# Performance work log

Measured on AMD Instinct MI355X. Metric: run time of the kernel, lower is better.

## Reference

```python
import jax, jax.numpy as jnp
import numpy as np

N, E, G = 32768, 262144, 1024
FIN, ED = 32, 8
H, C = 4, 64            # gat_heads, graph_hidden_dim
HC = H * C              # 256
FP_IN, DESC_IN = 2048, 200
GOUT, FPOUT, DOUT = 64, 256, 64
TIN = GOUT + FPOUT + DOUT  # 384
NT = 12
BN_EPS = 1e-5


def bn_eval(x, gamma, beta):
    # eval-mode BatchNorm1d with default running stats (mean=0, var=1)
    inv = 1.0 / jnp.sqrt(1.0 + BN_EPS)
    return x * (gamma * inv) + beta


def gatv2(x, edge_index, edge_attr, Wl, bl, Wr, br, We, att, bias):
    """PyG GATv2Conv (concat heads, add_self_loops=True, fill_value='mean')."""
    n = x.shape[0]
    src, dst = edge_index[0], edge_index[1]
    # self-loop edge_attr = mean of incoming edge_attr per node (PyG fill_value='mean')
    deg = jax.ops.segment_sum(jnp.ones(src.shape, x.dtype), dst, n)
    ea_loop = jax.ops.segment_sum(edge_attr, dst, n) / jnp.maximum(deg, 1.0)[:, None]
    loop = jnp.arange(n)
    src = jnp.concatenate([src, loop])
    dst = jnp.concatenate([dst, loop])
    ea = jnp.concatenate([edge_attr, ea_loop], axis=0)
    xl = (x @ Wl + bl).reshape(n, H, C)   # source transform
    xr = (x @ Wr + br).reshape(n, H, C)   # target transform
    ee = (ea @ We).reshape(-1, H, C)      # edge transform (no bias in PyG)
    m = jax.nn.leaky_relu(xl[src] + xr[dst] + ee, 0.2)  # [E', H, C]
    logit = jnp.einsum('ehc,hc->eh', m, att)            # [E', H]
    # segment softmax over incoming edges of each target node
    lmax = jax.ops.segment_max(logit, dst, n)
    p = jnp.exp(logit - lmax[dst])
    alpha = p / jax.ops.segment_sum(p, dst, n)[dst]
    out = jax.ops.segment_sum(xl[src] * alpha[:, :, None], dst, n)  # [n, H, C]
    return out.reshape(n, HC) + bias


def setup_inputs() -> dict:
    key = jax.random.key(0)
    ks = iter(jax.random.split(key, 64))

    def p(shape, scale=0.05):
        return jax.random.normal(next(ks), shape, dtype=jnp.float32) * scale

    inp = {}
    inp['x'] = jax.random.normal(next(ks), (N, FIN), dtype=jnp.float32)
    inp['edge_index'] = jax.random.randint(next(ks), (2, E), 0, N, dtype=jnp.int32)
    inp['edge_attr'] = jax.random.normal(next(ks), (E, ED), dtype=jnp.float32)
    inp['batch'] = (jnp.arange(N) * G) // N          # sorted, covers all G graphs
    inp['fp'] = jax.random.uniform(next(ks), (G, FP_IN), dtype=jnp.float32)
    inp['desc'] = jax.random.normal(next(ks), (G, DESC_IN), dtype=jnp.float32)
    # GATv2 layer 1 (in=FIN) and layer 2 (in=HC)
    for tag, fin in (('c1', FIN), ('c2', HC)):
        inp[tag + '_Wl'] = p((fin, HC))
        inp[tag + '_bl'] = p((HC,))
        inp[tag + '_Wr'] = p((fin, HC))
        inp[tag + '_br'] = p((HC,))
        inp[tag + '_We'] = p((ED, HC))
        inp[tag + '_att'] = p((H, C))
        inp[tag + '_bias'] = p((HC,))
    inp['gW'], inp['gb'] = p((HC, GOUT)), p((GOUT,))
    inp['g_gn'], inp['g_bt'] = jnp.ones((GOUT,)), jnp.zeros((GOUT,))
    inp['fW'], inp['fb'] = p((FP_IN, FPOUT)), p((FPOUT,))
    inp['f_gn'], inp['f_bt'] = jnp.ones((FPOUT,)), jnp.zeros((FPOUT,))
    inp['dW'], inp['db'] = p((DESC_IN, DOUT)), p((DOUT,))
    inp['d_gn'], inp['d_bt'] = jnp.ones((DOUT,)), jnp.zeros((DOUT,))
    inp['k1W'], inp['k1b'] = p((TIN, TIN // 2)), p((TIN // 2,))
    inp['k1_gn'], inp['k1_bt'] = jnp.ones((TIN // 2,)), jnp.zeros((TIN // 2,))
    inp['k2W'], inp['k2b'] = p((TIN // 2, TIN // 4)), p((TIN // 4,))
    inp['k2_gn'], inp['k2_bt'] = jnp.ones((TIN // 4,)), jnp.zeros((TIN // 4,))
    inp['k3W'], inp['k3b'] = p((TIN // 4, NT)), p((NT,))
    return inp


def reference(x, edge_index, edge_attr, batch, fp, desc,
              c1_Wl, c1_bl, c1_Wr, c1_br, c1_We, c1_att, c1_bias,
              c2_Wl, c2_bl, c2_Wr, c2_br, c2_We, c2_att, c2_bias,
              gW, gb, g_gn, g_bt, fW, fb, f_gn, f_bt, dW, db, d_gn, d_bt,
              k1W, k1b, k1_gn, k1_bt, k2W, k2b, k2_gn, k2_bt, k3W, k3b):
    h = jax.nn.relu(gatv2(x, edge_index, edge_attr, c1_Wl, c1_bl, c1_Wr, c1_br, c1_We, c1_att, c1_bias))
    h = jax.nn.relu(gatv2(h, edge_index, edge_attr, c2_Wl, c2_bl, c2_Wr, c2_br, c2_We, c2_att, c2_bias))
    xg = jax.ops.segment_max(h, batch, G)                 # global_max_pool
    xg = bn_eval(jax.nn.relu(xg @ gW + gb), g_gn, g_bt)
    xf = bn_eval(jax.nn.relu(fp @ fW + fb), f_gn, f_bt)
    xd = bn_eval(jax.nn.relu(desc @ dW + db), d_gn, d_bt)
    z = jnp.concatenate([xg, xf, xd], axis=1)             # [G, TIN]
    z = bn_eval(jax.nn.relu(z @ k1W + k1b), k1_gn, k1_bt)  # dropout off (eval)
    z = bn_eval(jax.nn.relu(z @ k2W + k2b), k2_gn, k2_bt)
    return z @ k3W + k3b                                  # [G, NT]
```

## Files before the change

### kernel.cpp

```cpp
#include <hip/hip_runtime.h>
#include <hip/hip_bf16.h>
#include <math.h>

#define NHEAD 4
#define HC 256

typedef short short8 __attribute__((ext_vector_type(8)));
typedef short short4v __attribute__((ext_vector_type(4)));
typedef float f32x4 __attribute__((ext_vector_type(4)));

__device__ inline f32x4 bf4_to_f32(short4v v)
{
  f32x4 r;
#pragma unroll
  for (int i = 0; i < 4; ++i)
    r[i] = __uint_as_float(((unsigned)(unsigned short)v[i]) << 16);
  return r;
}

__device__ inline float bf_to_f32(unsigned short u)
{
  return __uint_as_float(((unsigned)u) << 16);
}

template <int CTRL>
__device__ inline float dpp_radd(float x)
{
  int yi = __builtin_amdgcn_update_dpp(0, __float_as_int(x), CTRL, 0xf, 0xf, true);
  return x + __int_as_float(yi);
}

__global__ void prep_kernel(
    const float* __restrict__ x, const float* __restrict__ fp,
    const float* __restrict__ c1Wl, const float* __restrict__ c1Wr,
    const float* __restrict__ c2Wl, const float* __restrict__ c2Wr,
    const float* __restrict__ desc, const float* __restrict__ dW,
    const float* __restrict__ k1W,
    const int* __restrict__ dst, int* __restrict__ deg,
    __hip_bfloat16* __restrict__ xbf, __hip_bfloat16* __restrict__ fpbf,
    __hip_bfloat16* __restrict__ wt1, __hip_bfloat16* __restrict__ wt2,
    __hip_bfloat16* __restrict__ descbf, __hip_bfloat16* __restrict__ dwt,
    __hip_bfloat16* __restrict__ k1wt,
    int N, int G, int E, int DIN)
{
  const int n0 = N * 32, n1 = G * 2048, n2 = 512 * 32, n3 = 512 * 256;
  const int n4 = G * 224, n5 = 64 * 224, n6 = 192 * 384;
  int idx = blockIdx.x * 256 + threadIdx.x;
  if (idx < n0) { xbf[idx] = __float2bfloat16(x[idx]); return; }
  idx -= n0;
  if (idx < n1) { fpbf[idx] = __float2bfloat16(fp[idx]); return; }
  idx -= n1;
  if (idx < n2) {
    int n = idx / 32, k = idx - n * 32;
    float v = (n < 256) ? c1Wl[k * 256 + n] : c1Wr[k * 256 + (n - 256)];
    wt1[idx] = __float2bfloat16(v); return;
  }
  idx -= n2;
  if (idx < n3) {
    int n = idx / 256, k = idx - n * 256;
    float v = (n < 256) ? c2Wl[k * 256 + n] : c2Wr[k * 256 + (n - 256)];
    wt2[idx] = __float2bfloat16(v); return;
  }
  idx -= n3;
  if (idx < n4) {
    int row = idx / 224, kp = idx - row * 224;
    float v = (kp < DIN) ? desc[(long)row * DIN + kp] : 0.f;
    descbf[idx] = __float2bfloat16(v); return;
  }
  idx -= n4;
  if (idx < n5) {
    int n = idx / 224, kp = idx - n * 224;
    float v = (kp < DIN) ? dW[kp * 64 + n] : 0.f;
    dwt[idx] = __float2bfloat16(v); return;
  }
  idx -= n5;
  if (idx < n6) {
    int n = idx / 384, k = idx - n * 384;
    k1wt[idx] = __float2bfloat16(k1W[k * 192 + n]); return;
  }
  idx -= n6;
  if (idx < E) atomicAdd(&deg[dst[idx]], 1);
}

__global__ __launch_bounds__(256) void transpose_fwt_kernel(
    const float* __restrict__ fW, __hip_bfloat16* __restrict__ fwt)
{
  __shared__ float tile[64][65];
  int bk = blockIdx.x * 64, bn = blockIdx.y * 64;
  int tx = threadIdx.x & 63, ty = threadIdx.x >> 6;
#pragma unroll
  for (int j = 0; j < 16; ++j) {
    int kl = ty + j * 4;
    tile[kl][tx] = fW[(long)(bk + kl) * 256 + bn + tx];
  }
  __syncthreads();
#pragma unroll
  for (int j = 0; j < 16; ++j) {
    int nl = ty + j * 4;
    fwt[(long)(bn + nl) * 2048 + bk + tx] = __float2bfloat16(tile[tx][nl]);
  }
}

__global__ __launch_bounds__(256) void gemm_mfma_kernel(
    const __hip_bfloat16* __restrict__ A, const __hip_bfloat16* __restrict__ BT,
    const float* __restrict__ bl, const float* __restrict__ br,
    __hip_bfloat16* __restrict__ XL, __hip_bfloat16* __restrict__ XR, int M, int K)
{
  __shared__ short As[128 * 40];
  __shared__ short Bs[128 * 40];
  int bm = blockIdx.x * 128, bn = blockIdx.y * 128;
  int t = threadIdx.x;
  int w = t >> 6, l = t & 63;
  int quad = l >> 4, l16 = l & 15;
  int srow = t >> 1, scol = (t & 1) * 16;

  f32x4 acc[2][8];
#pragma unroll
  for (int i = 0; i < 2; ++i)
#pragma unroll
    for (int j = 0; j < 8; ++j) acc[i][j] = (f32x4){0.f, 0.f, 0.f, 0.f};

  for (int k0 = 0; k0 < K; k0 += 32) {
    *(short8*)&As[srow * 40 + scol] =
        *(const short8*)(const void*)&A[(long)(bm + srow) * K + k0 + scol];
    *(short8*)&As[srow * 40 + scol + 8] =
        *(const short8*)(const void*)&A[(long)(bm + srow) * K + k0 + scol + 8];
    *(short8*)&Bs[srow * 40 + scol] =
        *(const short8*)(const void*)&BT[(long)(bn + srow) * K + k0 + scol];
    *(short8*)&Bs[srow * 40 + scol + 8] =
        *(const short8*)(const void*)&BT[(long)(bn + srow) * K + k0 + scol + 8];
    __syncthreads();
    short8 af[2], bf[8];
#pragma unroll
    for (int mt = 0; mt < 2; ++mt)
      af[mt] = *(short8*)&As[(w * 32 + mt * 16 + l16) * 40 + quad * 8];
#pragma unroll
    for (int nt = 0; nt < 8; ++nt)
      bf[nt] = *(short8*)&Bs[(nt * 16 + l16) * 40 + quad * 8];
#pragma unroll
    for (int mt = 0; mt < 2; ++mt)
#pragma unroll
      for (int nt = 0; nt < 8; ++nt)
        acc[mt][nt] = __builtin_amdgcn_mfma_f32_16x16x32_bf16(af[mt], bf[nt], acc[mt][nt], 0, 0, 0);
    __syncthreads();
  }
#pragma unroll
  for (int mt = 0; mt < 2; ++mt)
#pragma unroll
    for (int nt = 0; nt < 8; ++nt) {
      int col = bn + nt * 16 + l16;
      float b = (col < 256) ? bl[col] : br[col - 256];
#pragma unroll
      for (int r = 0; r < 4; ++r) {
        int row = bm + w * 32 + mt * 16 + quad * 4 + r;
        float v = acc[mt][nt][r] + b;
        if (col < 256)
          XL[(long)row * 256 + col] = __float2bfloat16(v);
        else
          XR[(long)row * 256 + (col - 256)] = __float2bfloat16(v);
      }
    }
}

__global__ __launch_bounds__(256) void gemm_rb_kernel(
    const __hip_bfloat16* __restrict__ A, const __hip_bfloat16* __restrict__ BT,
    const float* __restrict__ bias, const float* __restrict__ gamma,
    const float* __restrict__ beta, void* __restrict__ out,
    int M, int K, int ldc, int coloff, int obf)
{
  __shared__ short As[64 * 40];
  __shared__ short Bs[64 * 40];
  int bm = blockIdx.x * 64, bn = blockIdx.y * 64;
  int t = threadIdx.x;
  int w = t >> 6, l = t & 63;
  int quad = l >> 4, l16 = l & 15;
  int lrow = t >> 2, col8 = (t & 3) * 8;

  f32x4 acc[4];
#pragma unroll
  for (int nt = 0; nt < 4; ++nt) acc[nt] = (f32x4){0.f, 0.f, 0.f, 0.f};

  for (int k0 = 0; k0 < K; k0 += 32) {
    *(short8*)&As[lrow * 40 + col8] =
        *(const short8*)(const void*)&A[(long)(bm + lrow) * K + k0 + col8];
    *(short8*)&Bs[lrow * 40 + col8] =
        *(const short8*)(const void*)&BT[(long)(bn + lrow) * K + k0 + col8];
    __syncthreads();
    short8 af = *(short8*)&As[(w * 16 + l16) * 40 + quad * 8];
#pragma unroll
    for (int nt = 0; nt < 4; ++nt) {
      short8 bf = *(short8*)&Bs[(nt * 16 + l16) * 40 + quad * 8];
      acc[nt] = __builtin_amdgcn_mfma_f32_16x16x32_bf16(af, bf, acc[nt], 0, 0, 0);
    }
    __syncthreads();
  }
  const float inv = rsqrtf(1.f + 1e-5f);
#pragma unroll
  for (int nt = 0; nt < 4; ++nt) {
    int col = bn + nt * 16 + l16;
    float b = bias[col], gm = gamma[col] * inv, bt = beta[col];
#pragma unroll
    for (int r = 0; r < 4; ++r) {
      int row = bm + w * 16 + quad * 4 + r;
      float v = fmaxf(acc[nt][r] + b, 0.f) * gm + bt;
      if (obf)
        ((__hip_bfloat16*)out)[(long)row * ldc + coloff + col] = __float2bfloat16(v);
      else
        ((float*)out)[(long)row * ldc + coloff + col] = v;
    }
  }
}

__global__ __launch_bounds__(256) void gemm_skb_kernel(
    const __hip_bfloat16* __restrict__ A, const __hip_bfloat16* __restrict__ BT,
    float* __restrict__ P, int M, int N, int K, int Kc)
{
  __shared__ short As[64 * 40];
  __shared__ short Bs[64 * 40];
  int bm = blockIdx.x * 64, bn = blockIdx.y * 64;
  int s = blockIdx.z;
  int kb = s * Kc, ke = kb + Kc;
  int t = threadIdx.x;
  int w = t >> 6, l = t & 63;
  int quad = l >> 4, l16 = l & 15;
  int lrow = t >> 2, col8 = (t & 3) * 8;

  f32x4 acc[4];
#pragma unroll
  for (int nt = 0; nt < 4; ++nt) acc[nt] = (f32x4){0.f, 0.f, 0.f, 0.f};

  for (int k0 = kb; k0 < ke; k0 += 32) {
    *(short8*)&As[lrow * 40 + col8] =
        *(const short8*)(const void*)&A[(long)(bm + lrow) * K + k0 + col8];
    *(short8*)&Bs[lrow * 40 + col8] =
        *(const short8*)(const void*)&BT[(long)(bn + lrow) * K + k0 + col8];
    __syncthreads();
    short8 af = *(short8*)&As[(w * 16 + l16) * 40 + quad * 8];
#pragma unroll
    for (int nt = 0; nt < 4; ++nt) {
      short8 bf = *(short8*)&Bs[(nt * 16 + l16) * 40 + quad * 8];
      acc[nt] = __builtin_amdgcn_mfma_f32_16x16x32_bf16(af, bf, acc[nt], 0, 0, 0);
    }
    __syncthreads();
  }
#pragma unroll
  for (int nt = 0; nt < 4; ++nt) {
    int col = bn + nt * 16 + l16;
#pragma unroll
    for (int r = 0; r < 4; ++r) {
      int row = bm + w * 16 + quad * 4 + r;
      P[((long)s * M + row) * N + col] = acc[nt][r];
    }
  }
}

__global__ __launch_bounds__(256) void fp_epilogue_kernel(
    const float* __restrict__ P, const float* __restrict__ bias,
    const float* __restrict__ gamma, const float* __restrict__ beta,
    __hip_bfloat16* __restrict__ zbuf, int M, int N, int S)
{
  int idx = blockIdx.x * 256 + threadIdx.x;
  if (idx >= M * N) return;
  int row = idx / N, col = idx - row * N;
  float v = 0.f;
  for (int s = 0; s < S; ++s) v += P[(long)s * M * N + idx];
  const float inv = rsqrtf(1.f + 1e-5f);
  v = fmaxf(v + bias[col], 0.f) * (gamma[col] * inv) + beta[col];
  zbuf[(long)row * 384 + 64 + col] = __float2bfloat16(v);
}

__global__ __launch_bounds__(256) void poolg_kernel(
    const __hip_bfloat16* __restrict__ h, const float* __restrict__ gW,
    const float* __restrict__ gb, const float* __restrict__ g_gn,
    const float* __restrict__ g_bt, __hip_bfloat16* __restrict__ zbuf, int npg)
{
  __shared__ float smax[256];
  __shared__ float sred[256];
  int g = blockIdx.x, t = threadIdx.x;
  const __hip_bfloat16* base = h + (long)g * npg * HC + t;
  float m = -INFINITY;
#pragma unroll 4
  for (int i = 0; i < npg; ++i)
    m = fmaxf(m, bf_to_f32(*(const unsigned short*)&base[(long)i * HC]));
  smax[t] = m;
  __syncthreads();
  int j = t >> 2, part = t & 3;
  float sum = 0.f;
#pragma unroll 4
  for (int k = part * 64; k < part * 64 + 64; ++k)
    sum = fmaf(smax[k], gW[k * 64 + j], sum);
  sred[t] = sum;
  __syncthreads();
  if (t < 64) {
    float v = sred[t * 4] + sred[t * 4 + 1] + sred[t * 4 + 2] + sred[t * 4 + 3];
    const float inv = rsqrtf(1.f + 1e-5f);
    v = fmaxf(v + gb[t], 0.f) * (g_gn[t] * inv) + g_bt[t];
    zbuf[(long)g * 384 + t] = __float2bfloat16(v);
  }
}

__global__ __launch_bounds__(256) void head23_kernel(
    const float* __restrict__ z1, const float* __restrict__ k2W,
    const float* __restrict__ k2b, const float* __restrict__ k2_gn,
    const float* __restrict__ k2_bt, const float* __restrict__ k3W,
    const float* __restrict__ k3b, float* __restrict__ out)
{
  __shared__ float s1[16 * 192];
  __shared__ float s2[16 * 96];
  int b = blockIdx.x, t = threadIdx.x;
  for (int i = t; i < 16 * 192; i += 256) s1[i] = z1[(long)b * 16 * 192 + i];
  __syncthreads();
  const float inv = rsqrtf(1.f + 1e-5f);
#pragma unroll
  for (int j = 0; j < 6; ++j) {
    int idx = j * 256 + t;
    int row = idx / 96, col = idx - row * 96;
    float acc = 0.f;
#pragma unroll 4
    for (int k = 0; k < 192; ++k) acc = fmaf(s1[row * 192 + k], k2W[k * 96 + col], acc);
    acc = fmaxf(acc + k2b[col], 0.f);
    s2[idx] = acc * (k2_gn[col] * inv) + k2_bt[col];
  }
  __syncthreads();
  if (t < 192) {
    int row = t / 12, col = t - row * 12;
    float acc = 0.f;
#pragma unroll 4
    for (int k = 0; k < 96; ++k) acc = fmaf(s2[row * 96 + k], k3W[k * 12 + col], acc);
    out[(long)(b * 16 + row) * 12 + col] = acc + k3b[col];
  }
}

__global__ __launch_bounds__(1024) void scan1_kernel(
    const int* __restrict__ deg, int* __restrict__ ptr,
    int* __restrict__ bsum, int N)
{
  __shared__ int s[1024];
  int b = blockIdx.x, t = threadIdx.x;
  int i = b * 1024 + t;
  int v = (i < N) ? deg[i] : 0;
  s[t] = v;
  __syncthreads();
  for (int off = 1; off < 1024; off <<= 1) {
    int x = (t >= off) ? s[t - off] : 0;
    __syncthreads();
    s[t] += x;
    __syncthreads();
  }
  if (i < N) ptr[i] = s[t] - v;
  if (t == 1023) bsum[b] = s[1023];
}

__global__ __launch_bounds__(256) void scan2_kernel(
    const int* __restrict__ bsum, int* __restrict__ ptr,
    int* __restrict__ cursor, int N, int nb)
{
  int i = blockIdx.x * 256 + threadIdx.x;
  if (i > N) return;
  if (i == N) {
    int tot = 0;
    for (int j = 0; j < nb; ++j) tot += bsum[j];
    ptr[N] = tot;
    return;
  }
  int b = i >> 10;
  int offv = 0;
  for (int j = 0; j < b; ++j) offv += bsum[j];
  int v = ptr[i] + offv;
  ptr[i] = v;
  cursor[i] = v;
}

__global__ void fill_kernel(const int* __restrict__ src, const int* __restrict__ dst,
                            const float* __restrict__ ea, int* __restrict__ cursor,
                            int* __restrict__ csr_src, float* __restrict__ csr_ea, int E)
{
  int e = blockIdx.x * blockDim.x + threadIdx.x;
  if (e < E) {
    int pos = atomicAdd(&cursor[dst[e]], 1);
    csr_src[pos] = src[e];
    f32x4 a0 = *(const f32x4*)(const void*)&ea[(long)e * 8];
    f32x4 a1 = *(const f32x4*)(const void*)&ea[(long)e * 8 + 4];
    *(f32x4*)&csr_ea[(long)pos * 8] = a0;
    *(f32x4*)&csr_ea[(long)pos * 8 + 4] = a1;
  }
}

__global__ __launch_bounds__(256) void eamean_kernel(
    const float* __restrict__ csr_ea, const int* __restrict__ csr_ptr,
    float* __restrict__ ea_mean, int N)
{
  int idx = blockIdx.x * 256 + threadIdx.x;
  if (idx >= N * 8) return;
  int node = idx >> 3, d = idx & 7;
  int p0 = csr_ptr[node], p1 = csr_ptr[node + 1];
  float s = 0.f;
  for (int k = p0; k < p1; ++k) s += csr_ea[(long)k * 8 + d];
  int cnt = p1 - p0;
  ea_mean[idx] = s / (float)(cnt > 1 ? cnt : 1);
}

__global__ __launch_bounds__(128) void gat_kernel(
    const __hip_bfloat16* __restrict__ xlb, const __hip_bfloat16* __restrict__ xrb,
    const float* __restrict__ csr_ea, const int* __restrict__ csr_src,
    const int* __restrict__ csr_ptr, const float* __restrict__ ea_mean,
    const float* __restrict__ We, const float* __restrict__ att,
    const float* __restrict__ bias, __hip_bfloat16* __restrict__ out, int N)
{
  int lane = threadIdx.x & 63;
  int node = blockIdx.x * 2 + (threadIdx.x >> 6);
  if (node >= N) return;
  int cbase = (lane >> 4) * 64 + (lane & 15) * 4;

  f32x4 attv = *(const f32x4*)(const void*)&att[cbase];
  f32x4 xriv = bf4_to_f32(*(const short4v*)(const void*)&xrb[(long)node * HC + cbase]);
  f32x4 WeR[8];
#pragma unroll
  for (int d = 0; d < 8; ++d)
    WeR[d] = *(const f32x4*)(const void*)&We[d * HC + cbase];

  float rsumA = 0.f, rsumB = 0.f;
  f32x4 accA = (f32x4){0.f, 0.f, 0.f, 0.f};
  f32x4 accB = (f32x4){0.f, 0.f, 0.f, 0.f};

  int p0 = csr_ptr[node], p1 = csr_ptr[node + 1];

  auto edge_compute = [&](f32x4 xls, f32x4 ea0, f32x4 ea1,
                          float& rsum, f32x4& acc) {
    f32x4 mv = xriv + xls;
#pragma unroll
    for (int d = 0; d < 4; ++d) mv += WeR[d] * ea0[d];
#pragma unroll
    for (int d = 0; d < 4; ++d) mv += WeR[d + 4] * ea1[d];
    float t = 0.f;
#pragma unroll
    for (int r = 0; r < 4; ++r) {
      float m = mv[r];
      m = (m > 0.f) ? m : 0.2f * m;
      t = fmaf(m, attv[r], t);
    }
    t = dpp_radd<0x121>(t);
    t = dpp_radd<0x122>(t);
    t = dpp_radd<0x124>(t);
    t = dpp_radd<0x128>(t);
    float p = __expf(t);
    rsum += p;
    acc += p * xls;
  };

  short4v xA = (short4v){0, 0, 0, 0}, xB = xA, xC = xA;
  f32x4 a0A = (f32x4){0.f, 0.f, 0.f, 0.f}, a1A = a0A;
  f32x4 a0B = a0A, a1B = a0A, a0C = a0A, a1C = a0A;
  if (p0 < p1) {
    int s = csr_src[p0];
    a0A = *(const f32x4*)(const void*)&csr_ea[(long)p0 * 8];
    a1A = *(const f32x4*)(const void*)&csr_ea[(long)p0 * 8 + 4];
    xA = *(const short4v*)(const void*)&xlb[(long)s * HC + cbase];
  }
  if (p0 + 1 < p1) {
    int s = csr_src[p0 + 1];
    a0B = *(const f32x4*)(const void*)&csr_ea[(long)(p0 + 1) * 8];
    a1B = *(const f32x4*)(const void*)&csr_ea[(long)(p0 + 1) * 8 + 4];
    xB = *(const short4v*)(const void*)&xlb[(long)s * HC + cbase];
  }
  if (p0 + 2 < p1) {
    int s = csr_src[p0 + 2];
    a0C = *(const f32x4*)(const void*)&csr_ea[(long)(p0 + 2) * 8];
    a1C = *(const f32x4*)(const void*)&csr_ea[(long)(p0 + 2) * 8 + 4];
    xC = *(const short4v*)(const void*)&xlb[(long)s * HC + cbase];
  }
  int k = p0;
  for (; k + 3 <= p1; k += 3) {
    f32x4 e0 = a0A, e1 = a1A;
    short4v xc = xA;
    if (k + 3 < p1) {
      int s = csr_src[k + 3];
      a0A = *(const f32x4*)(const void*)&csr_ea[(long)(k + 3) * 8];
      a1A = *(const f32x4*)(const void*)&csr_ea[(long)(k + 3) * 8 + 4];
      xA = *(const short4v*)(const void*)&xlb[(long)s * HC + cbase];
    }
    edge_compute(bf4_to_f32(xc), e0, e1, rsumA, accA);

    e0 = a0B; e1 = a1B; xc = xB;
    if (k + 4 < p1) {
      int s = csr_src[k + 4];
      a0B = *(const f32x4*)(const void*)&csr_ea[(long)(k + 4) * 8];
      a1B = *(const f32x4*)(const void*)&csr_ea[(long)(k + 4) * 8 + 4];
      xB = *(const short4v*)(const void*)&xlb[(long)s * HC + cbase];
    }
    edge_compute(bf4_to_f32(xc), e0, e1, rsumB, accB);

    e0 = a0C; e1 = a1C; xc = xC;
    if (k + 5 < p1) {
      int s = csr_src[k + 5];
      a0C = *(const f32x4*)(const void*)&csr_ea[(long)(k + 5) * 8];
      a1C = *(const f32x4*)(const void*)&csr_ea[(long)(k + 5) * 8 + 4];
      xC = *(const short4v*)(const void*)&xlb[(long)s * HC + cbase];
    }
    edge_compute(bf4_to_f32(xc), e0, e1, rsumA, accA);
  }
  if (k < p1)     edge_compute(bf4_to_f32(xA), a0A, a1A, rsumA, accA);
  if (k + 1 < p1) edge_compute(bf4_to_f32(xB), a0B, a1B, rsumB, accB);

  f32x4 em0 = *(const f32x4*)(const void*)&ea_mean[(long)node * 8];
  f32x4 em1 = *(const f32x4*)(const void*)&ea_mean[(long)node * 8 + 4];
  f32x4 xls_self = bf4_to_f32(*(const short4v*)(const void*)&xlb[(long)node * HC + cbase]);
  edge_compute(xls_self, em0, em1, rsumB, accB);

  float invs = 1.f / (rsumA + rsumB);
  f32x4 biasv = *(const f32x4*)(const void*)&bias[cbase];
  short4v pk;
#pragma unroll
  for (int r = 0; r < 4; ++r) {
    float v = fmaxf((accA[r] + accB[r]) * invs + biasv[r], 0.f);
    __hip_bfloat16 hv = __float2bfloat16(v);
    pk[r] = *(short*)&hv;
  }
  *(short4v*)&out[(long)node * HC + cbase] = pk;
}

extern "C" void kernel_launch(void* const* d_in, const int* in_sizes, int n_in,
                              void* d_out, int out_size, void* d_ws, size_t ws_size,
                              hipStream_t stream)
{
  const float* x          = (const float*)d_in[0];
  const int*   edge_index = (const int*)d_in[1];
  const float* edge_attr  = (const float*)d_in[2];
  const float* fp         = (const float*)d_in[4];
  const float* desc       = (const float*)d_in[5];
  const float *c1_Wl = (const float*)d_in[6],  *c1_bl = (const float*)d_in[7],
              *c1_Wr = (const float*)d_in[8],  *c1_br = (const float*)d_in[9],
              *c1_We = (const float*)d_in[10], *c1_att = (const float*)d_in[11],
              *c1_bias = (const float*)d_in[12];
  const float *c2_Wl = (const float*)d_in[13], *c2_bl = (const float*)d_in[14],
              *c2_Wr = (const float*)d_in[15], *c2_br = (const float*)d_in[16],
              *c2_We = (const float*)d_in[17], *c2_att = (const float*)d_in[18],
              *c2_bias = (const float*)d_in[19];
  const float *gW = (const float*)d_in[20], *gb = (const float*)d_in[21],
              *g_gn = (const float*)d_in[22], *g_bt = (const float*)d_in[23];
  const float *fW = (const float*)d_in[24], *fb = (const float*)d_in[25],
              *f_gn = (const float*)d_in[26], *f_bt = (const float*)d_in[27];
  const float *dW = (const float*)d_in[28], *db = (const float*)d_in[29],
              *d_gn = (const float*)d_in[30], *d_bt = (const float*)d_in[31];
  const float *k1W = (const float*)d_in[32], *k1b = (const float*)d_in[33],
              *k1_gn = (const float*)d_in[34], *k1_bt = (const float*)d_in[35];
  const float *k2W = (const float*)d_in[36], *k2b = (const float*)d_in[37],
              *k2_gn = (const float*)d_in[38], *k2_bt = (const float*)d_in[39];
  const float *k3W = (const float*)d_in[40], *k3b = (const float*)d_in[41];

  const int N = in_sizes[0] / 32;
  const int E = in_sizes[1] / 2;
  const int G = in_sizes[4] / 2048;
  const int FIN = 32, FPIN = 2048;
  const int DIN = in_sizes[5] / G;

  char* ws = (char*)d_ws;
  size_t off = 0;
  auto alloc = [&](size_t bytes) {
    void* p = ws + off;
    off = (off + bytes + 255) & ~(size_t)255;
    return p;
  };
  __hip_bfloat16* xlb    = (__hip_bfloat16*)alloc((size_t)N * HC * 2);
  __hip_bfloat16* xrb    = (__hip_bfloat16*)alloc((size_t)N * HC * 2);
  __hip_bfloat16* hb1    = (__hip_bfloat16*)alloc((size_t)N * HC * 2);
  __hip_bfloat16* hb2    = (__hip_bfloat16*)alloc((size_t)N * HC * 2);
  __hip_bfloat16* xbf    = (__hip_bfloat16*)alloc((size_t)N * FIN * 2);
  __hip_bfloat16* fpbf   = (__hip_bfloat16*)alloc((size_t)G * FPIN * 2);
  __hip_bfloat16* wt1    = (__hip_bfloat16*)alloc((size_t)512 * FIN * 2);
  __hip_bfloat16* wt2    = (__hip_bfloat16*)alloc((size_t)512 * HC * 2);
  __hip_bfloat16* fwt    = (__hip_bfloat16*)alloc((size_t)256 * FPIN * 2);
  __hip_bfloat16* descbf = (__hip_bfloat16*)alloc((size_t)G * 224 * 2);
  __hip_bfloat16* dwt    = (__hip_bfloat16*)alloc((size_t)64 * 224 * 2);
  __hip_bfloat16* k1wt   = (__hip_bfloat16*)alloc((size_t)192 * 384 * 2);
  __hip_bfloat16* zbuf   = (__hip_bfloat16*)alloc((size_t)G * 384 * 2);
  float* z1      = (float*)alloc((size_t)G * 192 * 4);
  float* P_fp    = (float*)alloc((size_t)4 * G * 256 * 4);
  int*   deg     = (int*)alloc((size_t)N * 4);
  int*   csr_ptr = (int*)alloc((size_t)(N + 1) * 4);
  int*   cursor  = (int*)alloc((size_t)N * 4);
  int*   csr_src = (int*)alloc((size_t)E * 4);
  float* csr_ea  = (float*)alloc((size_t)E * 8 * 4);
  float* ea_mean = (float*)alloc((size_t)N * 8 * 4);
  int*   bsum    = (int*)alloc((size_t)64 * 4);
  (void)ws_size;

  const int* srcp = edge_index;
  const int* dstp = edge_index + E;
  const int nb = (N + 1023) / 1024;

  hipMemsetAsync(deg, 0, (size_t)N * 4, stream);

  {
    long total = (long)N * FIN + (long)G * FPIN + 512 * 32 + 512 * 256 +
                 (long)G * 224 + 64 * 224 + 192 * 384 + E;
    prep_kernel<<<(int)((total + 255) / 256), 256, 0, stream>>>(
        x, fp, c1_Wl, c1_Wr, c2_Wl, c2_Wr, desc, dW, k1W, dstp, deg,
        xbf, fpbf, wt1, wt2, descbf, dwt, k1wt, N, G, E, DIN);
  }
  transpose_fwt_kernel<<<dim3(2048 / 64, 256 / 64), 256, 0, stream>>>(fW, fwt);
  scan1_kernel<<<nb, 1024, 0, stream>>>(deg, csr_ptr, bsum, N);
  scan2_kernel<<<(N + 1 + 255) / 256, 256, 0, stream>>>(bsum, csr_ptr, cursor, N, nb);
  fill_kernel<<<(E + 255) / 256, 256, 0, stream>>>(srcp, dstp, edge_attr, cursor,
                                                   csr_src, csr_ea, E);
  eamean_kernel<<<(N * 8 + 255) / 256, 256, 0, stream>>>(csr_ea, csr_ptr, ea_mean, N);

  gemm_skb_kernel<<<dim3(G / 64, 4, 4), 256, 0, stream>>>(fpbf, fwt, P_fp,
                                                          G, 256, FPIN, FPIN / 4);
  fp_epilogue_kernel<<<(G * 256 + 255) / 256, 256, 0, stream>>>(P_fp, fb, f_gn, f_bt,
                                                                zbuf, G, 256, 4);
  gemm_rb_kernel<<<dim3(G / 64, 1), 256, 0, stream>>>(descbf, dwt, db, d_gn, d_bt,
                                                      zbuf, G, 224, 384, 320, 1);

  gemm_mfma_kernel<<<dim3(N / 128, 4), 256, 0, stream>>>(xbf, wt1, c1_bl, c1_br, xlb, xrb, N, FIN);
  gat_kernel<<<N / 2, 128, 0, stream>>>(xlb, xrb, csr_ea, csr_src, csr_ptr, ea_mean,
                                        c1_We, c1_att, c1_bias, hb1, N);
  gemm_mfma_kernel<<<dim3(N / 128, 4), 256, 0, stream>>>(hb1, wt2, c2_bl, c2_br, xlb, xrb, N, HC);
  gat_kernel<<<N / 2, 128, 0, stream>>>(xlb, xrb, csr_ea, csr_src, csr_ptr, ea_mean,
                                        c2_We, c2_att, c2_bias, hb2, N);

  poolg_kernel<<<G, 256, 0, stream>>>(hb2, gW, gb, g_gn, g_bt, zbuf, N / G);

  gemm_rb_kernel<<<dim3(G / 64, 3), 256, 0, stream>>>(zbuf, k1wt, k1b, k1_gn, k1_bt,
                                                      z1, G, 384, 192, 0, 0);
  head23_kernel<<<G / 16, 256, 0, stream>>>(z1, k2W, k2b, k2_gn, k2_bt, k3W, k3b,
                                            (float*)d_out);
}
```

Before: 450.4 us.

## Process two nodes per wavefront in GAT and fold edge-attr mean into fill

```diff
diff --git a/kernel.cpp b/kernel.cpp
--- a/kernel.cpp
+++ b/kernel.cpp
@@ -373,60 +373,60 @@
 
 __global__ void fill_kernel(const int* __restrict__ src, const int* __restrict__ dst,
                             const float* __restrict__ ea, int* __restrict__ cursor,
-                            int* __restrict__ csr_src, float* __restrict__ csr_ea, int E)
+                            int* __restrict__ csr_src, float* __restrict__ csr_ea,
+                            float* __restrict__ ea_sum, int E)
 {
   int e = blockIdx.x * blockDim.x + threadIdx.x;
   if (e < E) {
-    int pos = atomicAdd(&cursor[dst[e]], 1);
+    int d = dst[e];
+    int pos = atomicAdd(&cursor[d], 1);
     csr_src[pos] = src[e];
     f32x4 a0 = *(const f32x4*)(const void*)&ea[(long)e * 8];
     f32x4 a1 = *(const f32x4*)(const void*)&ea[(long)e * 8 + 4];
     *(f32x4*)&csr_ea[(long)pos * 8] = a0;
     *(f32x4*)&csr_ea[(long)pos * 8 + 4] = a1;
-  }
-}
-
-__global__ __launch_bounds__(256) void eamean_kernel(
-    const float* __restrict__ csr_ea, const int* __restrict__ csr_ptr,
-    float* __restrict__ ea_mean, int N)
-{
-  int idx = blockIdx.x * 256 + threadIdx.x;
-  if (idx >= N * 8) return;
-  int node = idx >> 3, d = idx & 7;
-  int p0 = csr_ptr[node], p1 = csr_ptr[node + 1];
-  float s = 0.f;
-  for (int k = p0; k < p1; ++k) s += csr_ea[(long)k * 8 + d];
-  int cnt = p1 - p0;
-  ea_mean[idx] = s / (float)(cnt > 1 ? cnt : 1);
+#pragma unroll
+    for (int i = 0; i < 4; ++i) atomicAdd(&ea_sum[(long)d * 8 + i], a0[i]);
+#pragma unroll
+    for (int i = 0; i < 4; ++i) atomicAdd(&ea_sum[(long)d * 8 + 4 + i], a1[i]);
+  }
 }
 
 __global__ __launch_bounds__(128) void gat_kernel(
     const __hip_bfloat16* __restrict__ xlb, const __hip_bfloat16* __restrict__ xrb,
     const float* __restrict__ csr_ea, const int* __restrict__ csr_src,
-    const int* __restrict__ csr_ptr, const float* __restrict__ ea_mean,
+    const int* __restrict__ csr_ptr, const float* __restrict__ ea_sum,
     const float* __restrict__ We, const float* __restrict__ att,
     const float* __restrict__ bias, __hip_bfloat16* __restrict__ out, int N)
 {
   int lane = threadIdx.x & 63;
-  int node = blockIdx.x * 2 + (threadIdx.x >> 6);
-  if (node >= N) return;
+  int nodeX = blockIdx.x * 4 + (threadIdx.x >> 6) * 2;
+  int nodeY = nodeX + 1;
   int cbase = (lane >> 4) * 64 + (lane & 15) * 4;
 
+  int p0X = csr_ptr[nodeX], p0Y = csr_ptr[nodeY], p1Y = csr_ptr[nodeY + 1];
+  int degX = p0Y - p0X, degY = p1Y - p0Y;
+
+  short4v xXA = (short4v){0, 0, 0, 0}, xXB = xXA, xYA = xXA, xYB = xXA;
+  if (degX > 0) xXA = *(const short4v*)(const void*)&xlb[(long)csr_src[p0X] * HC + cbase];
+  if (degY > 0) xYA = *(const short4v*)(const void*)&xlb[(long)csr_src[p0Y] * HC + cbase];
+  if (degX > 1) xXB = *(const short4v*)(const void*)&xlb[(long)csr_src[p0X + 1] * HC + cbase];
+  if (degY > 1) xYB = *(const short4v*)(const void*)&xlb[(long)csr_src[p0Y + 1] * HC + cbase];
+
   f32x4 attv = *(const f32x4*)(const void*)&att[cbase];
-  f32x4 xriv = bf4_to_f32(*(const short4v*)(const void*)&xrb[(long)node * HC + cbase]);
+  f32x4 xrivX = bf4_to_f32(*(const short4v*)(const void*)&xrb[(long)nodeX * HC + cbase]);
+  f32x4 xrivY = bf4_to_f32(*(const short4v*)(const void*)&xrb[(long)nodeY * HC + cbase]);
   f32x4 WeR[8];
 #pragma unroll
   for (int d = 0; d < 8; ++d)
     WeR[d] = *(const f32x4*)(const void*)&We[d * HC + cbase];
 
-  float rsumA = 0.f, rsumB = 0.f;
-  f32x4 accA = (f32x4){0.f, 0.f, 0.f, 0.f};
-  f32x4 accB = (f32x4){0.f, 0.f, 0.f, 0.f};
-
-  int p0 = csr_ptr[node], p1 = csr_ptr[node + 1];
-
-  auto edge_compute = [&](f32x4 xls, f32x4 ea0, f32x4 ea1,
-                          float& rsum, f32x4& acc) {
+  float rsumX = 0.f, rsumY = 0.f;
+  f32x4 accX = (f32x4){0.f, 0.f, 0.f, 0.f};
+  f32x4 accY = (f32x4){0.f, 0.f, 0.f, 0.f};
+
+  auto ec = [&](f32x4 xriv, f32x4 xls, f32x4 ea0, f32x4 ea1,
+                float& rsum, f32x4& acc) {
     f32x4 mv = xriv + xls;
 #pragma unroll
     for (int d = 0; d < 4; ++d) mv += WeR[d] * ea0[d];
@@ -448,75 +448,84 @@
     acc += p * xls;
   };
 
-  short4v xA = (short4v){0, 0, 0, 0}, xB = xA, xC = xA;
-  f32x4 a0A = (f32x4){0.f, 0.f, 0.f, 0.f}, a1A = a0A;
-  f32x4 a0B = a0A, a1B = a0A, a0C = a0A, a1C = a0A;
-  if (p0 < p1) {
-    int s = csr_src[p0];
-    a0A = *(const f32x4*)(const void*)&csr_ea[(long)p0 * 8];
-    a1A = *(const f32x4*)(const void*)&csr_ea[(long)p0 * 8 + 4];
-    xA = *(const short4v*)(const void*)&xlb[(long)s * HC + cbase];
-  }
-  if (p0 + 1 < p1) {
-    int s = csr_src[p0 + 1];
-    a0B = *(const f32x4*)(const void*)&csr_ea[(long)(p0 + 1) * 8];
-    a1B = *(const f32x4*)(const void*)&csr_ea[(long)(p0 + 1) * 8 + 4];
-    xB = *(const short4v*)(const void*)&xlb[(long)s * HC + cbase];
-  }
-  if (p0 + 2 < p1) {
-    int s = csr_src[p0 + 2];
-    a0C = *(const f32x4*)(const void*)&csr_ea[(long)(p0 + 2) * 8];
-    a1C = *(const f32x4*)(const void*)&csr_ea[(long)(p0 + 2) * 8 + 4];
-    xC = *(const short4v*)(const void*)&xlb[(long)s * HC + cbase];
-  }
-  int k = p0;
-  for (; k + 3 <= p1; k += 3) {
-    f32x4 e0 = a0A, e1 = a1A;
-    short4v xc = xA;
-    if (k + 3 < p1) {
-      int s = csr_src[k + 3];
-      a0A = *(const f32x4*)(const void*)&csr_ea[(long)(k + 3) * 8];
-      a1A = *(const f32x4*)(const void*)&csr_ea[(long)(k + 3) * 8 + 4];
-      xA = *(const short4v*)(const void*)&xlb[(long)s * HC + cbase];
-    }
-    edge_compute(bf4_to_f32(xc), e0, e1, rsumA, accA);
-
-    e0 = a0B; e1 = a1B; xc = xB;
-    if (k + 4 < p1) {
-      int s = csr_src[k + 4];
-      a0B = *(const f32x4*)(const void*)&csr_ea[(long)(k + 4) * 8];
-      a1B = *(const f32x4*)(const void*)&csr_ea[(long)(k + 4) * 8 + 4];
-      xB = *(const short4v*)(const void*)&xlb[(long)s * HC + cbase];
-    }
-    edge_compute(bf4_to_f32(xc), e0, e1, rsumB, accB);
-
-    e0 = a0C; e1 = a1C; xc = xC;
-    if (k + 5 < p1) {
-      int s = csr_src[k + 5];
-      a0C = *(const f32x4*)(const void*)&csr_ea[(long)(k + 5) * 8];
-      a1C = *(const f32x4*)(const void*)&csr_ea[(long)(k + 5) * 8 + 4];
-      xC = *(const short4v*)(const void*)&xlb[(long)s * HC + cbase];
-    }
-    edge_compute(bf4_to_f32(xc), e0, e1, rsumA, accA);
-  }
-  if (k < p1)     edge_compute(bf4_to_f32(xA), a0A, a1A, rsumA, accA);
-  if (k + 1 < p1) edge_compute(bf4_to_f32(xB), a0B, a1B, rsumB, accB);
-
-  f32x4 em0 = *(const f32x4*)(const void*)&ea_mean[(long)node * 8];
-  f32x4 em1 = *(const f32x4*)(const void*)&ea_mean[(long)node * 8 + 4];
-  f32x4 xls_self = bf4_to_f32(*(const short4v*)(const void*)&xlb[(long)node * HC + cbase]);
-  edge_compute(xls_self, em0, em1, rsumB, accB);
-
-  float invs = 1.f / (rsumA + rsumB);
+  int dmax = degX > degY ? degX : degY;
+  int i = 0;
+  for (; i + 2 <= dmax; i += 2) {
+    if (i < degX) {
+      f32x4 e0 = *(const f32x4*)(const void*)&csr_ea[(long)(p0X + i) * 8];
+      f32x4 e1 = *(const f32x4*)(const void*)&csr_ea[(long)(p0X + i) * 8 + 4];
+      short4v xc = xXA;
+      if (i + 2 < degX)
+        xXA = *(const short4v*)(const void*)&xlb[(long)csr_src[p0X + i + 2] * HC + cbase];
+      ec(xrivX, bf4_to_f32(xc), e0, e1, rsumX, accX);
+    }
+    if (i < degY) {
+      f32x4 e0 = *(const f32x4*)(const void*)&csr_ea[(long)(p0Y + i) * 8];
+      f32x4 e1 = *(const f32x4*)(const void*)&csr_ea[(long)(p0Y + i) * 8 + 4];
+      short4v xc = xYA;
+      if (i + 2 < degY)
+        xYA = *(const short4v*)(const void*)&xlb[(long)csr_src[p0Y + i + 2] * HC + cbase];
+      ec(xrivY, bf4_to_f32(xc), e0, e1, rsumY, accY);
+    }
+    if (i + 1 < degX) {
+      f32x4 e0 = *(const f32x4*)(const void*)&csr_ea[(long)(p0X + i + 1) * 8];
+      f32x4 e1 = *(const f32x4*)(const void*)&csr_ea[(long)(p0X + i + 1) * 8 + 4];
+      short4v xc = xXB;
+      if (i + 3 < degX)
+        xXB = *(const short4v*)(const void*)&xlb[(long)csr_src[p0X + i + 3] * HC + cbase];
+      ec(xrivX, bf4_to_f32(xc), e0, e1, rsumX, accX);
+    }
+    if (i + 1 < degY) {
+      f32x4 e0 = *(const f32x4*)(const void*)&csr_ea[(long)(p0Y + i + 1) * 8];
+      f32x4 e1 = *(const f32x4*)(const void*)&csr_ea[(long)(p0Y + i + 1) * 8 + 4];
+      short4v xc = xYB;
+      if (i + 3 < degY)
+        xYB = *(const short4v*)(const void*)&xlb[(long)csr_src[p0Y + i + 3] * HC + cbase];
+      ec(xrivY, bf4_to_f32(xc), e0, e1, rsumY, accY);
+    }
+  }
+  if (dmax & 1) {
+    if (i < degX) {
+      f32x4 e0 = *(const f32x4*)(const void*)&csr_ea[(long)(p0X + i) * 8];
+      f32x4 e1 = *(const f32x4*)(const void*)&csr_ea[(long)(p0X + i) * 8 + 4];
+      ec(xrivX, bf4_to_f32(xXA), e0, e1, rsumX, accX);
+    }
+    if (i < degY) {
+      f32x4 e0 = *(const f32x4*)(const void*)&csr_ea[(long)(p0Y + i) * 8];
+      f32x4 e1 = *(const f32x4*)(const void*)&csr_ea[(long)(p0Y + i) * 8 + 4];
+      ec(xrivY, bf4_to_f32(xYA), e0, e1, rsumY, accY);
+    }
+  }
+
+  {
+    float invdX = 1.f / (float)(degX > 1 ? degX : 1);
+    f32x4 em0 = *(const f32x4*)(const void*)&ea_sum[(long)nodeX * 8];
+    f32x4 em1 = *(const f32x4*)(const void*)&ea_sum[(long)nodeX * 8 + 4];
+    f32x4 xs = bf4_to_f32(*(const short4v*)(const void*)&xlb[(long)nodeX * HC + cbase]);
+    ec(xrivX, xs, em0 * invdX, em1 * invdX, rsumX, accX);
+  }
+  {
+    float invdY = 1.f / (float)(degY > 1 ? degY : 1);
+    f32x4 em0 = *(const f32x4*)(const void*)&ea_sum[(long)nodeY * 8];
+    f32x4 em1 = *(const f32x4*)(const void*)&ea_sum[(long)nodeY * 8 + 4];
+    f32x4 xs = bf4_to_f32(*(const short4v*)(const void*)&xlb[(long)nodeY * HC + cbase]);
+    ec(xrivY, xs, em0 * invdY, em1 * invdY, rsumY, accY);
+  }
+
   f32x4 biasv = *(const f32x4*)(const void*)&bias[cbase];
-  short4v pk;
+  float invsX = 1.f / rsumX, invsY = 1.f / rsumY;
+  short4v pkX, pkY;
 #pragma unroll
   for (int r = 0; r < 4; ++r) {
-    float v = fmaxf((accA[r] + accB[r]) * invs + biasv[r], 0.f);
-    __hip_bfloat16 hv = __float2bfloat16(v);
-    pk[r] = *(short*)&hv;
-  }
-  *(short4v*)&out[(long)node * HC + cbase] = pk;
+    float vX = fmaxf(accX[r] * invsX + biasv[r], 0.f);
+    float vY = fmaxf(accY[r] * invsY + biasv[r], 0.f);
+    __hip_bfloat16 hX = __float2bfloat16(vX);
+    __hip_bfloat16 hY = __float2bfloat16(vY);
+    pkX[r] = *(short*)&hX;
+    pkY[r] = *(short*)&hY;
+  }
+  *(short4v*)&out[(long)nodeX * HC + cbase] = pkX;
+  *(short4v*)&out[(long)nodeY * HC + cbase] = pkY;
 }
 
 extern "C" void kernel_launch(void* const* d_in, const int* in_sizes, int n_in,
@@ -581,7 +590,7 @@
   int*   cursor  = (int*)alloc((size_t)N * 4);
   int*   csr_src = (int*)alloc((size_t)E * 4);
   float* csr_ea  = (float*)alloc((size_t)E * 8 * 4);
-  float* ea_mean = (float*)alloc((size_t)N * 8 * 4);
+  float* ea_sum  = (float*)alloc((size_t)N * 8 * 4);
   int*   bsum    = (int*)alloc((size_t)64 * 4);
   (void)ws_size;
 
@@ -590,6 +599,7 @@
   const int nb = (N + 1023) / 1024;
 
   hipMemsetAsync(deg, 0, (size_t)N * 4, stream);
+  hipMemsetAsync(ea_sum, 0, (size_t)N * 8 * 4, stream);
 
   {
     long total = (long)N * FIN + (long)G * FPIN + 512 * 32 + 512 * 256 +
@@ -602,8 +612,7 @@
   scan1_kernel<<<nb, 1024, 0, stream>>>(deg, csr_ptr, bsum, N);
   scan2_kernel<<<(N + 1 + 255) / 256, 256, 0, stream>>>(bsum, csr_ptr, cursor, N, nb);
   fill_kernel<<<(E + 255) / 256, 256, 0, stream>>>(srcp, dstp, edge_attr, cursor,
-                                                   csr_src, csr_ea, E);
-  eamean_kernel<<<(N * 8 + 255) / 256, 256, 0, stream>>>(csr_ea, csr_ptr, ea_mean, N);
+                                                   csr_src, csr_ea, ea_sum, E);
 
   gemm_skb_kernel<<<dim3(G / 64, 4, 4), 256, 0, stream>>>(fpbf, fwt, P_fp,
                                                           G, 256, FPIN, FPIN / 4);
@@ -613,10 +622,10 @@
                                                       zbuf, G, 224, 384, 320, 1);
 
   gemm_mfma_kernel<<<dim3(N / 128, 4), 256, 0, stream>>>(xbf, wt1, c1_bl, c1_br, xlb, xrb, N, FIN);
-  gat_kernel<<<N / 2, 128, 0, stream>>>(xlb, xrb, csr_ea, csr_src, csr_ptr, ea_mean,
+  gat_kernel<<<N / 4, 128, 0, stream>>>(xlb, xrb, csr_ea, csr_src, csr_ptr, ea_sum,
                                         c1_We, c1_att, c1_bias, hb1, N);
   gemm_mfma_kernel<<<dim3(N / 128, 4), 256, 0, stream>>>(hb1, wt2, c2_bl, c2_br, xlb, xrb, N, HC);
-  gat_kernel<<<N / 2, 128, 0, stream>>>(xlb, xrb, csr_ea, csr_src, csr_ptr, ea_mean,
+  gat_kernel<<<N / 4, 128, 0, stream>>>(xlb, xrb, csr_ea, csr_src, csr_ptr, ea_sum,
                                         c2_We, c2_att, c2_bias, hb2, N);
 
   poolg_kernel<<<G, 256, 0, stream>>>(hb2, gW, gb, g_gn, g_bt, zbuf, N / G);
```

After: 564.5 us. 1.25x slower.
